# Performance work log

Hardware: AMD Instinct MI355X
Metric: run time of the kernel (lower is better)

## Reference

```python
import jax, jax.numpy as jnp
import numpy as np

B, N = 2048, 2048

def setup_inputs() -> dict:
    key = jax.random.key(0)
    k1, k2, k3 = jax.random.split(key, 3)
    src_coords = jax.random.normal(k1, (B, N, 3), dtype=jnp.float32)
    tgt_coords = jax.random.normal(k2, (B, N, 3), dtype=jnp.float32)
    weights = jax.random.uniform(k3, (B, 1, N), dtype=jnp.float32)
    return {"src_coords": src_coords, "tgt_coords": tgt_coords, "weights": weights}

def reference(src_coords, tgt_coords, weights):
    # (b,N,3) -> (b,3,N), matching torch transpose(2,1)
    src = jnp.swapaxes(src_coords, 1, 2)
    tgt = jnp.swapaxes(tgt_coords, 1, 2)
    # total weight per batch (b,1,1)
    w = jnp.sum(weights, axis=2, keepdims=True) + 1e-4
    # weighted centroids (b,3,1)
    src_centroid = jnp.sum(src * weights, axis=2, keepdims=True) / w
    tgt_centroid = jnp.sum(tgt * weights, axis=2, keepdims=True) / w
    src_centered = src - src_centroid
    tgt_centered = tgt - tgt_centroid
    # weighted cross-covariance (b,3,3): bmm(tgt_centered*weights, src_centered^T)/w
    W = jnp.einsum('bin,bjn->bij', tgt_centered * weights, src_centered) / w
    U, _, Vh = jnp.linalg.svd(W)  # torch.svd returns V; Vh = V^T, det(V)=det(Vh)
    det_UV = jnp.linalg.det(U) * jnp.linalg.det(Vh)
    # S = diag(1, 1, det_UV)
    s = jnp.stack([jnp.ones_like(det_UV), jnp.ones_like(det_UV), det_UV], axis=-1)
    # R = U @ diag(s) @ V^T
    R_tgt_src = jnp.einsum('bij,bj,bjk->bik', U, s, Vh)
    # t_tgt_src_insrc = src_centroid - R^T @ tgt_centroid
    t_tgt_src_insrc = src_centroid - jnp.einsum('bji,bjk->bik', R_tgt_src, tgt_centroid)
    t_src_tgt_intgt = -jnp.einsum('bij,bjk->bik', R_tgt_src, t_tgt_src_insrc)
    return (R_tgt_src, t_src_tgt_intgt)
```

## Files before the change

kernel.cpp:

```cpp
#include <hip/hip_runtime.h>
#include <math.h>

#define B_BATCH 2048
#define N_PTS   2048

__global__ __launch_bounds__(256) void reduce_kernel(
    const float* __restrict__ src, const float* __restrict__ tgt,
    const float* __restrict__ wts, float* __restrict__ sums)
{
    const int bid  = blockIdx.x;
    const int b    = bid >> 1;
    const int half = bid & 1;
    const int tid  = threadIdx.x;

    const float4* s4 = (const float4*)(src + (size_t)b * N_PTS * 3) + half * 768;
    const float4* t4 = (const float4*)(tgt + (size_t)b * N_PTS * 3) + half * 768;
    const float4* w4 = (const float4*)(wts + (size_t)b * N_PTS) + half * 256;

    float4 sv[3], tv[3], wq;
#pragma unroll
    for (int k = 0; k < 3; ++k) sv[k] = s4[3 * tid + k];
#pragma unroll
    for (int k = 0; k < 3; ++k) tv[k] = t4[3 * tid + k];
    wq = w4[tid];

    const float* sf = (const float*)sv;
    const float* tf = (const float*)tv;
    const float* wf = (const float*)&wq;

    float acc[16];
#pragma unroll
    for (int i = 0; i < 16; ++i) acc[i] = 0.f;

#pragma unroll
    for (int p = 0; p < 4; ++p) {
        const float w  = wf[p];
        const float sx = sf[3*p+0], sy = sf[3*p+1], sz = sf[3*p+2];
        const float tx = tf[3*p+0], ty = tf[3*p+1], tz = tf[3*p+2];
        const float wsx = w * sx, wsy = w * sy, wsz = w * sz;
        acc[0]  += w;
        acc[1]  += wsx;      acc[2]  += wsy;      acc[3]  += wsz;
        acc[4]  += w * tx;   acc[5]  += w * ty;   acc[6]  += w * tz;
        acc[7]  += tx * wsx; acc[8]  += tx * wsy; acc[9]  += tx * wsz;
        acc[10] += ty * wsx; acc[11] += ty * wsy; acc[12] += ty * wsz;
        acc[13] += tz * wsx; acc[14] += tz * wsy; acc[15] += tz * wsz;
    }

#pragma unroll
    for (int i = 0; i < 16; ++i) {
#pragma unroll
        for (int off = 32; off > 0; off >>= 1)
            acc[i] += __shfl_down(acc[i], off, 64);
    }

    __shared__ float red[4][16];
    const int lane = tid & 63, wv_ = tid >> 6;
    if (lane == 0) {
#pragma unroll
        for (int i = 0; i < 16; ++i) red[wv_][i] = acc[i];
    }
    __syncthreads();
    if (tid < 16)
        sums[(size_t)bid * 16 + tid] =
            red[0][tid] + red[1][tid] + red[2][tid] + red[3][tid];
}

__global__ __launch_bounds__(64) void svd_kernel(
    const float* __restrict__ sums,
    float* __restrict__ outR, float* __restrict__ outT)
{
    const int b = blockIdx.x * blockDim.x + threadIdx.x;
    if (b >= B_BATCH) return;
    const float* P0 = sums + (size_t)b * 32;
    const float* P1 = P0 + 16;
    float S[16];
#pragma unroll
    for (int i = 0; i < 16; ++i) S[i] = P0[i] + P1[i];

    const double wtot = (double)S[0] + 1e-4;
    const double inv  = 1.0 / wtot;
    double sc[3] = { S[1]*inv, S[2]*inv, S[3]*inv };
    double tc[3] = { S[4]*inv, S[5]*inv, S[6]*inv };
    const double f = (wtot + 1e-4) * inv;

    double W[3][3];
#pragma unroll
    for (int i = 0; i < 3; ++i)
#pragma unroll
        for (int j = 0; j < 3; ++j)
            W[i][j] = (double)S[7 + 3*i + j] * inv - f * tc[i] * sc[j];

    double A[3][3];
    for (int i = 0; i < 3; ++i)
        for (int j = 0; j < 3; ++j) {
            double s = 0.0;
            for (int k = 0; k < 3; ++k) s += W[k][i] * W[k][j];
            A[i][j] = s;
        }

    double V[3][3] = {{1,0,0},{0,1,0},{0,0,1}};
    const double tr0 = fabs(A[0][0]) + fabs(A[1][1]) + fabs(A[2][2]) + 1e-300;
    for (int sweep = 0; sweep < 8; ++sweep) {
        double offd = fabs(A[0][1]) + fabs(A[0][2]) + fabs(A[1][2]);
        if (offd <= 1e-28 * tr0) break;
        for (int pq = 0; pq < 3; ++pq) {
            const int p = (pq == 2) ? 1 : 0;
            const int q = (pq == 0) ? 1 : 2;
            const double apq = A[p][q];
            if (fabs(apq) == 0.0) continue;
            const double tau = (A[q][q] - A[p][p]) / (2.0 * apq);
            const double tt  = (tau >= 0.0 ? 1.0 : -1.0) /
                               (fabs(tau) + sqrt(1.0 + tau * tau));
            const double c = 1.0 / sqrt(1.0 + tt * tt);
            const double s = tt * c;
            for (int k = 0; k < 3; ++k) {
                const double akp = A[k][p], akq = A[k][q];
                A[k][p] = c * akp - s * akq;
                A[k][q] = s * akp + c * akq;
            }
            for (int k = 0; k < 3; ++k) {
                const double apk = A[p][k], aqk = A[q][k];
                A[p][k] = c * apk - s * aqk;
                A[q][k] = s * apk + c * aqk;
            }
            for (int k = 0; k < 3; ++k) {
                const double vkp = V[k][p], vkq = V[k][q];
                V[k][p] = c * vkp - s * vkq;
                V[k][q] = s * vkp + c * vkq;
            }
        }
    }

    double lam[3] = { A[0][0], A[1][1], A[2][2] };
    int idx[3] = {0, 1, 2};
    if (lam[idx[0]] < lam[idx[1]]) { int t_ = idx[0]; idx[0] = idx[1]; idx[1] = t_; }
    if (lam[idx[0]] < lam[idx[2]]) { int t_ = idx[0]; idx[0] = idx[2]; idx[2] = t_; }
    if (lam[idx[1]] < lam[idx[2]]) { int t_ = idx[1]; idx[1] = idx[2]; idx[2] = t_; }

    double v[3][3];
#pragma unroll
    for (int c = 0; c < 3; ++c)
        for (int r = 0; r < 3; ++r) v[r][c] = V[r][idx[c]];

    double u[3][3];
    double col[3];
    for (int r = 0; r < 3; ++r)
        col[r] = W[r][0]*v[0][0] + W[r][1]*v[1][0] + W[r][2]*v[2][0];
    double s0 = sqrt(col[0]*col[0] + col[1]*col[1] + col[2]*col[2]);
    if (s0 > 1e-150) {
        for (int r = 0; r < 3; ++r) u[r][0] = col[r] / s0;
    } else {
        u[0][0] = 1.0; u[1][0] = 0.0; u[2][0] = 0.0;
    }
    for (int r = 0; r < 3; ++r)
        col[r] = W[r][0]*v[0][1] + W[r][1]*v[1][1] + W[r][2]*v[2][1];
    {
        double d01 = col[0]*u[0][0] + col[1]*u[1][0] + col[2]*u[2][0];
        for (int r = 0; r < 3; ++r) col[r] -= d01 * u[r][0];
        double s1 = sqrt(col[0]*col[0] + col[1]*col[1] + col[2]*col[2]);
        if (s1 > 1e-12 * (1.0 + s0)) {
            for (int r = 0; r < 3; ++r) u[r][1] = col[r] / s1;
        } else {
            double ax = fabs(u[0][0]), ay = fabs(u[1][0]), az = fabs(u[2][0]);
            double e[3] = {0, 0, 0};
            if (ax <= ay && ax <= az) e[0] = 1.0;
            else if (ay <= az)        e[1] = 1.0;
            else                      e[2] = 1.0;
            double p0 = u[1][0]*e[2] - u[2][0]*e[1];
            double p1 = u[2][0]*e[0] - u[0][0]*e[2];
            double p2 = u[0][0]*e[1] - u[1][0]*e[0];
            double pn = sqrt(p0*p0 + p1*p1 + p2*p2);
            u[0][1] = p0/pn; u[1][1] = p1/pn; u[2][1] = p2/pn;
        }
    }
    for (int r = 0; r < 3; ++r)
        col[r] = W[r][0]*v[0][2] + W[r][1]*v[1][2] + W[r][2]*v[2][2];
    {
        double d02 = col[0]*u[0][0] + col[1]*u[1][0] + col[2]*u[2][0];
        double d12 = col[0]*u[0][1] + col[1]*u[1][1] + col[2]*u[2][1];
        for (int r = 0; r < 3; ++r) col[r] -= d02 * u[r][0] + d12 * u[r][1];
        double s2 = sqrt(col[0]*col[0] + col[1]*col[1] + col[2]*col[2]);
        if (s2 > 1e-12 * (1.0 + s0)) {
            for (int r = 0; r < 3; ++r) u[r][2] = col[r] / s2;
        } else {
            u[0][2] = u[1][0]*u[2][1] - u[2][0]*u[1][1];
            u[1][2] = u[2][0]*u[0][1] - u[0][0]*u[2][1];
            u[2][2] = u[0][0]*u[1][1] - u[1][0]*u[0][1];
        }
    }

    double detU =
        u[0][0]*(u[1][1]*u[2][2] - u[2][1]*u[1][2]) -
        u[0][1]*(u[1][0]*u[2][2] - u[2][0]*u[1][2]) +
        u[0][2]*(u[1][0]*u[2][1] - u[2][0]*u[1][1]);
    double detV =
        v[0][0]*(v[1][1]*v[2][2] - v[2][1]*v[1][2]) -
        v[0][1]*(v[1][0]*v[2][2] - v[2][0]*v[1][2]) +
        v[0][2]*(v[1][0]*v[2][1] - v[2][0]*v[1][1]);
    const double d = (detU * detV >= 0.0) ? 1.0 : -1.0;

    double R[3][3];
#pragma unroll
    for (int r = 0; r < 3; ++r)
#pragma unroll
        for (int c = 0; c < 3; ++c)
            R[r][c] = u[r][0]*v[c][0] + u[r][1]*v[c][1] + d * u[r][2]*v[c][2];

    float* Rb = outR + (size_t)b * 9;
#pragma unroll
    for (int r = 0; r < 3; ++r)
#pragma unroll
        for (int c = 0; c < 3; ++c)
            Rb[3*r + c] = (float)R[r][c];

    float* Tb = outT + (size_t)b * 3;
#pragma unroll
    for (int r = 0; r < 3; ++r)
        Tb[r] = (float)(tc[r] - (R[r][0]*sc[0] + R[r][1]*sc[1] + R[r][2]*sc[2]));
}

extern "C" void kernel_launch(void* const* d_in, const int* in_sizes, int n_in,
                              void* d_out, int out_size, void* d_ws, size_t ws_size,
                              hipStream_t stream) {
    const float* src = (const float*)d_in[0];
    const float* tgt = (const float*)d_in[1];
    const float* wts = (const float*)d_in[2];
    float* outR = (float*)d_out;
    float* outT = outR + (size_t)B_BATCH * 9;
    float* sums = (float*)d_ws;

    reduce_kernel<<<B_BATCH * 2, 256, 0, stream>>>(src, tgt, wts, sums);
    svd_kernel<<<B_BATCH / 64, 64, 0, stream>>>(sums, outR, outT);
}
```

Measured before the change: 142.9 us.

## Fuse reduction and SVD via last-block atomic counter with XCD-aware block remap

Merges the reduction and per-batch SVD kernels into one launch: each block writes its partial sums, bumps a per-batch atomic counter, and whichever of the two half-blocks finishes second runs the 3x3 SVD on a single thread. A small kernel zeroes the counters first. Block indices are remapped so consecutive physical blocks spread across the 8 XCDs, and launch bounds now request two blocks per CU. This removes the separate SVD kernel's launch and its serial tail, but a lone double-precision thread per block doing the Jacobi SVD could lengthen block lifetime and raise register pressure.

```diff
diff --git a/kernel.cpp b/kernel.cpp
--- a/kernel.cpp
+++ b/kernel.cpp
@@ -4,11 +4,20 @@
 #define B_BATCH 2048
 #define N_PTS   2048
 
-__global__ __launch_bounds__(256) void reduce_kernel(
+#define CTR_OFF (B_BATCH * 32)
+
+__global__ __launch_bounds__(256) void zero_counters(int* __restrict__ C) {
+    const int i = blockIdx.x * blockDim.x + threadIdx.x;
+    if (i < B_BATCH) C[i] = 0;
+}
+
+__global__ __launch_bounds__(256, 2) void reduce_svd_kernel(
     const float* __restrict__ src, const float* __restrict__ tgt,
-    const float* __restrict__ wts, float* __restrict__ sums)
+    const float* __restrict__ wts, float* __restrict__ ws,
+    float* __restrict__ outR, float* __restrict__ outT)
 {
-    const int bid  = blockIdx.x;
+    const int phys = blockIdx.x;
+    const int bid  = (phys & 7) * 512 + (phys >> 3);
     const int b    = bid >> 1;
     const int half = bid & 1;
     const int tid  = threadIdx.x;
@@ -61,21 +70,22 @@
     }
     __syncthreads();
     if (tid < 16)
-        sums[(size_t)bid * 16 + tid] =
+        ws[(size_t)b * 32 + half * 16 + tid] =
             red[0][tid] + red[1][tid] + red[2][tid] + red[3][tid];
-}
-
-__global__ __launch_bounds__(64) void svd_kernel(
-    const float* __restrict__ sums,
-    float* __restrict__ outR, float* __restrict__ outT)
-{
-    const int b = blockIdx.x * blockDim.x + threadIdx.x;
-    if (b >= B_BATCH) return;
-    const float* P0 = sums + (size_t)b * 32;
-    const float* P1 = P0 + 16;
+    __syncthreads();
+
+    if (tid != 0) return;
+
+    __threadfence();
+    int* ctr = (int*)(ws + CTR_OFF);
+    const int old = atomicAdd(&ctr[b], 1);
+    if (old != 1) return;
+    __threadfence();
+
+    const float* P = ws + (size_t)b * 32;
     float S[16];
 #pragma unroll
-    for (int i = 0; i < 16; ++i) S[i] = P0[i] + P1[i];
+    for (int i = 0; i < 16; ++i) S[i] = P[i] + P[16 + i];
 
     const double wtot = (double)S[0] + 1e-4;
     const double inv  = 1.0 / wtot;
@@ -227,8 +237,8 @@
     const float* wts = (const float*)d_in[2];
     float* outR = (float*)d_out;
     float* outT = outR + (size_t)B_BATCH * 9;
-    float* sums = (float*)d_ws;
-
-    reduce_kernel<<<B_BATCH * 2, 256, 0, stream>>>(src, tgt, wts, sums);
-    svd_kernel<<<B_BATCH / 64, 64, 0, stream>>>(sums, outR, outT);
+    float* ws   = (float*)d_ws;
+
+    zero_counters<<<(B_BATCH + 255) / 256, 256, 0, stream>>>((int*)(ws + CTR_OFF));
+    reduce_svd_kernel<<<B_BATCH * 2, 256, 0, stream>>>(src, tgt, wts, ws, outR, outT);
 }
```

Result: slower. 432.5 us (+202.8%).
